# Optimization experiments

Hardware: AMD Instinct MI355X
Metric: run time of the kernel (lower is better)

The kernel has to match this reference:

```python
import jax, jax.numpy as jnp
import numpy as np

N_NODES = 200000
N_EDGES = 800000
N_MOL = 10000
IN_DIM, HDIM, EDGE_DIM = 40, 64, 16
BN_EPS = 1e-5


def _bn_eval(h, gamma, beta, mean, var):
    # BatchNorm1d in eval mode (running stats)
    return gamma * (h - mean) * jax.lax.rsqrt(var + BN_EPS) + beta


def _gine(x, src, dst, edge_attr, We, be, W, b, gamma, beta, mean, var):
    # GINEConv (eps=0): agg_i = sum_{(j->i)} relu(x_j + lin_e(e_ji)); h = nn(x + agg)
    msg = jax.nn.relu(x[src] + edge_attr @ We.T + be)          # [E, d]
    agg = jax.ops.segment_sum(msg, dst, num_segments=x.shape[0])
    h = (x + agg) @ W.T + b                                    # Linear
    h = _bn_eval(h, gamma, beta, mean, var)                    # BatchNorm1d
    return jax.nn.leaky_relu(h)                                # LeakyReLU(0.01); Dropout is identity in eval


def setup_inputs() -> dict:
    key = jax.random.key(0)
    ks = jax.random.split(key, 40)
    d = {}
    d['x'] = jax.random.normal(ks[0], (N_NODES, IN_DIM), jnp.float32)
    d['edge_index'] = jax.random.randint(ks[1], (2, N_EDGES), 0, N_NODES, jnp.int32)
    d['edge_attr'] = jax.random.normal(ks[2], (N_EDGES, EDGE_DIM), jnp.float32)
    d['batch'] = jnp.sort(jax.random.randint(ks[3], (N_NODES,), 0, N_MOL, jnp.int32))
    i = 4
    def nrm(shape, scale=0.05):
        nonlocal i
        i += 1
        return jax.random.normal(ks[i - 1], shape, jnp.float32) * scale
    for l, din in ((1, IN_DIM), (2, HDIM), (3, HDIM)):
        d[f'We{l}'] = nrm((din, EDGE_DIM)); d[f'be{l}'] = nrm((din,))
        d[f'W{l}'] = nrm((HDIM, din)); d[f'b{l}'] = nrm((HDIM,))
        d[f'g{l}'] = jnp.ones((HDIM,), jnp.float32); d[f'bb{l}'] = jnp.zeros((HDIM,), jnp.float32)
        d[f'm{l}'] = nrm((HDIM,)); d[f'v{l}'] = jax.random.uniform(ks[i], (HDIM,), jnp.float32, 0.5, 1.5); i += 1
    D4 = 4 * HDIM
    d['Wl1'] = nrm((D4, D4)); d['bl1'] = nrm((D4,))
    d['Wl2'] = nrm((1, D4)); d['bl2'] = nrm((1,))
    return d


def reference(x, edge_index, edge_attr, batch,
              We1, be1, W1, b1, g1, bb1, m1, v1,
              We2, be2, W2, b2, g2, bb2, m2, v2,
              We3, be3, W3, b3, g3, bb3, m3, v3,
              Wl1, bl1, Wl2, bl2):
    src, dst = edge_index[0], edge_index[1]
    h1 = _gine(x, src, dst, edge_attr, We1, be1, W1, b1, g1, bb1, m1, v1)
    h2 = _gine(h1, src, dst, edge_attr, We2, be2, W2, b2, g2, bb2, m2, v2)
    h3 = _gine(h2, src, dst, edge_attr, We3, be3, W3, b3, g3, bb3, m3, v3)
    h_pool = jax.ops.segment_sum(h3, batch, num_segments=N_MOL)   # global_add_pool
    h_pool_ = h_pool[batch]                                       # repeat_interleave by per-mol counts
    h = jnp.concatenate([h1, h2, h3, h_pool_], axis=1)            # [N, 4*hdim]
    h = jax.nn.leaky_relu(h @ Wl1.T + bl1)
    return h @ Wl2.T + bl2                                        # [N, 1]
```

## Files before the change

kernel.cpp:

```cpp
#include <hip/hip_runtime.h>
#include <hip/hip_bf16.h>

#define N_NODES 200000
#define N_EDGES 800000
#define N_MOL   10000
#define HDIM    64
#define EDGE_DIM 16
#define BN_EPS 1e-5f
#define SCAN_BLOCKS ((N_NODES + 255) / 256)

typedef __attribute__((ext_vector_type(8))) short short8;
typedef __attribute__((ext_vector_type(4))) float f32x4;

__device__ __forceinline__ unsigned int pk2(float a, float b) {
    __hip_bfloat162 h = __float22bfloat162_rn(make_float2(a, b));
    union { __hip_bfloat162 h; unsigned int u; } c;
    c.h = h;
    return c.u;
}
__device__ __forceinline__ short8 cvt8(float4 a, float4 b) {
    union { short8 s; unsigned int u[4]; } r;
    r.u[0] = pk2(a.x, a.y); r.u[1] = pk2(a.z, a.w);
    r.u[2] = pk2(b.x, b.y); r.u[3] = pk2(b.z, b.w);
    return r.s;
}
__device__ __forceinline__ float bf2f(unsigned short u) {
    return __uint_as_float(((unsigned int)u) << 16);
}
__device__ __forceinline__ unsigned short f2bf(float a) {
    union { __hip_bfloat16 h; unsigned short u; } c;
    c.h = __float2bfloat16(a);
    return c.u;
}
__device__ __forceinline__ float4 bf4f(ushort4 u) {
    return make_float4(bf2f(u.x), bf2f(u.y), bf2f(u.z), bf2f(u.w));
}

__global__ __launch_bounds__(256) void cvtx_kernel(
    const float* __restrict__ x, unsigned short* __restrict__ xb)
{
    int i = blockIdx.x * 256 + threadIdx.x;
    if ((size_t)i * 4 >= (size_t)N_NODES * 40) return;
    float4 v = *(const float4*)(x + (size_t)i * 4);
    union { ushort4 s; unsigned int u[2]; } r;
    r.u[0] = pk2(v.x, v.y); r.u[1] = pk2(v.z, v.w);
    *(ushort4*)(xb + (size_t)i * 4) = r.s;
}

__global__ __launch_bounds__(256) void hist_kernel(
    const int* __restrict__ ei, int* __restrict__ counts)
{
    int e = blockIdx.x * 256 + threadIdx.x;
    if (e < N_EDGES) atomicAdd(&counts[ei[N_EDGES + e]], 1);
}

__global__ __launch_bounds__(256) void scan_phase_a(
    const int* __restrict__ counts,
    int* __restrict__ row_ptr, int* __restrict__ block_sums)
{
    __shared__ int lds[256];
    int t = threadIdx.x;
    int i = blockIdx.x * 256 + t;
    int v = (i < N_NODES) ? counts[i] : 0;
    lds[t] = v;
    __syncthreads();
    for (int off = 1; off < 256; off <<= 1) {
        int u = (t >= off) ? lds[t - off] : 0;
        __syncthreads();
        lds[t] += u;
        __syncthreads();
    }
    if (i < N_NODES) row_ptr[i] = lds[t] - v;
    if (t == 255) block_sums[blockIdx.x] = lds[255];
}

__global__ __launch_bounds__(1024) void scan_phase_b(
    int* __restrict__ block_sums)
{
    __shared__ int lds[1024];
    int t = threadIdx.x;
    int v = (t < SCAN_BLOCKS) ? block_sums[t] : 0;
    lds[t] = v;
    __syncthreads();
    for (int off = 1; off < 1024; off <<= 1) {
        int u = (t >= off) ? lds[t - off] : 0;
        __syncthreads();
        lds[t] += u;
        __syncthreads();
    }
    if (t < SCAN_BLOCKS) block_sums[t] = lds[t] - v;
}

__global__ __launch_bounds__(256) void scan_phase_c(
    const int* __restrict__ block_sums,
    int* __restrict__ row_ptr, int* __restrict__ cursor)
{
    int i = blockIdx.x * 256 + threadIdx.x;
    if (i < N_NODES) {
        int v = row_ptr[i] + block_sums[blockIdx.x];
        row_ptr[i] = v;
        cursor[i] = v;
    }
    if (i == 0) row_ptr[N_NODES] = N_EDGES;
}

__global__ __launch_bounds__(256) void scatter_kernel(
    const int* __restrict__ ei, int* __restrict__ cursor,
    int* __restrict__ src_sorted, int* __restrict__ eid_sorted)
{
    int e = blockIdx.x * 256 + threadIdx.x;
    if (e >= N_EDGES) return;
    int d = ei[N_EDGES + e];
    int pos = atomicAdd(&cursor[d], 1);
    src_sorted[pos] = ei[e];
    eid_sorted[pos] = e;
}

#define EMSG_WAVES 8192
template<int DIN>
__global__ __launch_bounds__(256) void emsg_mfma(
    const float* __restrict__ ea,
    const int*   __restrict__ eid_sorted,
    const float* __restrict__ We,
    const float* __restrict__ be,
    unsigned short* __restrict__ emsg)
{
    constexpr int NFT = (DIN + 15) / 16;
    int lane = threadIdx.x & 63;
    int wv = blockIdx.x * 4 + (threadIdx.x >> 6);
    int r = lane & 15, g = lane >> 4;
    const short8 zero8 = (short8){0, 0, 0, 0, 0, 0, 0, 0};

    short8 af[NFT];
    float4 bb[NFT];
    bool   sv[NFT];
#pragma unroll
    for (int ft = 0; ft < NFT; ft++) {
        int feat = ft * 16 + r;
        if (g < 2 && feat < DIN) {
            const float4* w4 = (const float4*)(We + feat * 16 + g * 8);
            af[ft] = cvt8(w4[0], w4[1]);
        } else {
            af[ft] = zero8;
        }
        int feat0 = ft * 16 + g * 4;
        sv[ft] = (feat0 < DIN);
        bb[ft] = sv[ft] ? *(const float4*)(be + feat0)
                        : make_float4(0.f, 0.f, 0.f, 0.f);
    }

    const int NT = N_EDGES / 16;
#pragma unroll 1
    for (int tile = wv; tile < NT; tile += EMSG_WAVES) {
        int j0 = tile * 16;
        int e = eid_sorted[j0 + r];
        short8 zf = zero8;
        if (g < 2) {
            const float4* ep = (const float4*)(ea + (size_t)e * 16 + g * 8);
            zf = cvt8(ep[0], ep[1]);
        }
#pragma unroll
        for (int ft = 0; ft < NFT; ft++) {
            f32x4 acc = (f32x4){0.f, 0.f, 0.f, 0.f};
            acc = __builtin_amdgcn_mfma_f32_16x16x32_bf16(af[ft], zf, acc, 0, 0, 0);
            if (sv[ft]) {
                ushort4 st;
                st.x = f2bf(acc[0] + bb[ft].x);
                st.y = f2bf(acc[1] + bb[ft].y);
                st.z = f2bf(acc[2] + bb[ft].z);
                st.w = f2bf(acc[3] + bb[ft].w);
                *(ushort4*)(emsg + (size_t)(j0 + r) * DIN + ft * 16 + g * 4) = st;
            }
        }
    }
}

template<int DIN>
__global__ __launch_bounds__(256) void agg_pre(
    const unsigned short* __restrict__ feat,
    const int*   __restrict__ row_ptr,
    const int*   __restrict__ src_sorted,
    const unsigned short* __restrict__ emsg,
    unsigned short* __restrict__ AGGb)
{
    int lane = threadIdx.x & 63;
    int wv = blockIdx.x * 4 + (threadIdx.x >> 6);
    int n0 = wv * 8;
    if (n0 >= N_NODES) return;
    int eg = lane >> 4;
    int f4 = lane & 15;
    const bool vf = (f4 * 4 < DIN);
    const int f4c = vf ? f4 : 0;

    int lo = row_ptr[n0];
#pragma unroll 1
    for (int ni = 0; ni < 8; ni++) {
        int node = n0 + ni;
        int hi = row_ptr[node + 1];
        float4 acc = {0.f, 0.f, 0.f, 0.f};
#pragma unroll 1
        for (int j0 = lo; j0 < hi; j0 += 4) {
            int j = j0 + eg;
            bool ev = (j < hi);
            int jc = ev ? j : (hi - 1);
            int s = src_sorted[jc];
            ushort4 xu = *(const ushort4*)(feat + (size_t)s * DIN + f4c * 4);
            ushort4 mu = *(const ushort4*)(emsg + (size_t)jc * DIN + f4c * 4);
            float4 xv = bf4f(xu), mv = bf4f(mu);
            float t0 = fmaxf(xv.x + mv.x, 0.f);
            float t1 = fmaxf(xv.y + mv.y, 0.f);
            float t2 = fmaxf(xv.z + mv.z, 0.f);
            float t3 = fmaxf(xv.w + mv.w, 0.f);
            if (ev && vf) {
                acc.x += t0; acc.y += t1; acc.z += t2; acc.w += t3;
            }
        }
        acc.x += __shfl_xor(acc.x, 16, 64);
        acc.y += __shfl_xor(acc.y, 16, 64);
        acc.z += __shfl_xor(acc.z, 16, 64);
        acc.w += __shfl_xor(acc.w, 16, 64);
        acc.x += __shfl_xor(acc.x, 32, 64);
        acc.y += __shfl_xor(acc.y, 32, 64);
        acc.z += __shfl_xor(acc.z, 32, 64);
        acc.w += __shfl_xor(acc.w, 32, 64);
        if (eg == 0) {
            float4 xd = {0.f, 0.f, 0.f, 0.f};
            if (vf) xd = bf4f(*(const ushort4*)(feat + (size_t)node * DIN + f4 * 4));
            float4 o = vf ? make_float4(acc.x + xd.x, acc.y + xd.y,
                                        acc.z + xd.z, acc.w + xd.w)
                          : make_float4(0.f, 0.f, 0.f, 0.f);
            ushort4 st;
            st.x = f2bf(o.x); st.y = f2bf(o.y);
            st.z = f2bf(o.z); st.w = f2bf(o.w);
            *(ushort4*)(AGGb + (size_t)node * HDIM + f4 * 4) = st;
        }
        lo = hi;
    }
}

template<int DIN>
__global__ __launch_bounds__(256) void agg_kernel(
    const unsigned short* __restrict__ feat,
    const int*   __restrict__ row_ptr,
    const int*   __restrict__ src_sorted,
    const int*   __restrict__ eid_sorted,
    const float* __restrict__ ea,
    const float* __restrict__ We,
    const float* __restrict__ be,
    unsigned short* __restrict__ AGGb)
{
    int lane = threadIdx.x & 63;
    int wv = __builtin_amdgcn_readfirstlane(blockIdx.x * 4 + (threadIdx.x >> 6));
    int n0 = wv * 8;
    if (n0 >= N_NODES) return;
    int f = lane;

    float wrow[16];
    float bias = 0.f;
    if (f < DIN) {
#pragma unroll
        for (int j = 0; j < 16; j++) wrow[j] = We[f * 16 + j];
        bias = be[f];
    } else {
#pragma unroll
        for (int j = 0; j < 16; j++) wrow[j] = 0.f;
    }

    int lo = row_ptr[n0];
    int hi = row_ptr[n0 + 8];
    int cur = 0;
    int nb = row_ptr[n0 + 1];
    float acc = 0.f;

    for (int j0 = lo; j0 < hi; j0 += 8) {
        int jn = min(8, hi - j0);
        int s[8], e[8];
#pragma unroll
        for (int k = 0; k < 8; k++) {
            int j = min(j0 + k, hi - 1);
            s[k] = src_sorted[j];
            e[k] = eid_sorted[j];
        }
        float xv[8];
#pragma unroll
        for (int k = 0; k < 8; k++)
            xv[k] = (f < DIN) ? bf2f(feat[(size_t)s[k] * DIN + f]) : 0.f;

#pragma unroll
        for (int k = 0; k < 8; k++) {
            if (k >= jn) break;
            int j = j0 + k;
            while (j >= nb) {
                float xd = (f < DIN) ? bf2f(feat[(size_t)(n0 + cur) * DIN + f]) : 0.f;
                AGGb[(size_t)(n0 + cur) * HDIM + f] = f2bf(acc + xd);
                acc = 0.f;
                cur++;
                nb = row_ptr[n0 + cur + 1];
            }
            const float4* ep = (const float4*)(ea + (size_t)e[k] * 16);
            float4 q0 = ep[0], q1 = ep[1], q2 = ep[2], q3 = ep[3];
            float a = bias;
            a = fmaf(q0.x, wrow[0],  a); a = fmaf(q0.y, wrow[1],  a);
            a = fmaf(q0.z, wrow[2],  a); a = fmaf(q0.w, wrow[3],  a);
            a = fmaf(q1.x, wrow[4],  a); a = fmaf(q1.y, wrow[5],  a);
            a = fmaf(q1.z, wrow[6],  a); a = fmaf(q1.w, wrow[7],  a);
            a = fmaf(q2.x, wrow[8],  a); a = fmaf(q2.y, wrow[9],  a);
            a = fmaf(q2.z, wrow[10], a); a = fmaf(q2.w, wrow[11], a);
            a = fmaf(q3.x, wrow[12], a); a = fmaf(q3.y, wrow[13], a);
            a = fmaf(q3.z, wrow[14], a); a = fmaf(q3.w, wrow[15], a);
            acc += fmaxf(xv[k] + a, 0.f);
        }
    }
    while (cur < 8) {
        float xd = (f < DIN) ? bf2f(feat[(size_t)(n0 + cur) * DIN + f]) : 0.f;
        AGGb[(size_t)(n0 + cur) * HDIM + f] = f2bf(acc + xd);
        acc = 0.f;
        cur++;
    }
}

template<int DIN>
__global__ __launch_bounds__(256) void node_mfma(
    const unsigned short* __restrict__ AGGb,
    unsigned short* __restrict__ Hb,
    const float* __restrict__ W,
    const float* __restrict__ bias,
    const float* __restrict__ gam,
    const float* __restrict__ bet,
    const float* __restrict__ mean,
    const float* __restrict__ var)
{
    int lane = threadIdx.x & 63;
    int wave = blockIdx.x * 4 + (threadIdx.x >> 6);
    if (wave >= N_NODES / 64) return;
    int n0 = wave * 64;
    int r = lane & 15;
    int g = lane >> 4;

    const short8 zero8 = (short8){0, 0, 0, 0, 0, 0, 0, 0};

    short8 zf[4][2];
#pragma unroll
    for (int nt = 0; nt < 4; nt++) {
        int node = n0 + nt * 16 + r;
        const unsigned short* ar = AGGb + (size_t)node * HDIM;
        zf[nt][0] = *(const short8*)(ar + g * 8);
        zf[nt][1] = *(const short8*)(ar + 32 + g * 8);
    }

    const float4* b4  = (const float4*)bias;
    const float4* g4  = (const float4*)gam;
    const float4* be4 = (const float4*)bet;
    const float4* m4  = (const float4*)mean;
    const float4* v4  = (const float4*)var;

#pragma unroll
    for (int ft = 0; ft < 4; ft++) {
        const float* wr = W + (size_t)(ft * 16 + r) * DIN;
        short8 af[2];
        {
            float4 w0 = *(const float4*)(wr + g * 8);
            float4 w1 = *(const float4*)(wr + g * 8 + 4);
            af[0] = cvt8(w0, w1);
            if (DIN == 64) {
                w0 = *(const float4*)(wr + 32 + g * 8);
                w1 = *(const float4*)(wr + 36 + g * 8);
                af[1] = cvt8(w0, w1);
            } else if (g == 0) {
                w0 = *(const float4*)(wr + 32);
                w1 = *(const float4*)(wr + 36);
                af[1] = cvt8(w0, w1);
            } else {
                af[1] = zero8;
            }
        }

        f32x4 acc[4];
#pragma unroll
        for (int nt = 0; nt < 4; nt++) acc[nt] = (f32x4){0.f, 0.f, 0.f, 0.f};

#pragma unroll
        for (int ks = 0; ks < 2; ks++) {
#pragma unroll
            for (int nt = 0; nt < 4; nt++) {
                acc[nt] = __builtin_amdgcn_mfma_f32_16x16x32_bf16(
                    af[ks], zf[nt][ks], acc[nt], 0, 0, 0);
            }
        }

        int idx = ft * 4 + g;
        float4 bb = b4[idx], gg = g4[idx], bt = be4[idx], mm = m4[idx], vv = v4[idx];
        float s0 = gg.x * rsqrtf(vv.x + BN_EPS);
        float s1 = gg.y * rsqrtf(vv.y + BN_EPS);
        float s2 = gg.z * rsqrtf(vv.z + BN_EPS);
        float s3 = gg.w * rsqrtf(vv.w + BN_EPS);
#pragma unroll
        for (int nt = 0; nt < 4; nt++) {
            int node = n0 + nt * 16 + r;
            float y0 = s0 * (acc[nt][0] + bb.x - mm.x) + bt.x;
            float y1 = s1 * (acc[nt][1] + bb.y - mm.y) + bt.y;
            float y2 = s2 * (acc[nt][2] + bb.z - mm.z) + bt.z;
            float y3 = s3 * (acc[nt][3] + bb.w - mm.w) + bt.w;
            y0 = (y0 > 0.f) ? y0 : 0.01f * y0;
            y1 = (y1 > 0.f) ? y1 : 0.01f * y1;
            y2 = (y2 > 0.f) ? y2 : 0.01f * y2;
            y3 = (y3 > 0.f) ? y3 : 0.01f * y3;
            union { uint2 v; unsigned int u[2]; } st;
            st.u[0] = pk2(y0, y1);
            st.u[1] = pk2(y2, y3);
            *(uint2*)(Hb + (size_t)node * HDIM + ft * 16 + g * 4) = st.v;
        }
    }
}

__global__ __launch_bounds__(256) void pool_kernel(
    const unsigned short* __restrict__ h3b,
    const int*   __restrict__ batch,
    float*       __restrict__ hpool)
{
    int gid = blockIdx.x * 256 + threadIdx.x;
    if (gid >= N_NODES * HDIM) return;
    int i = gid >> 6, f = gid & 63;
    atomicAdd(&hpool[(size_t)batch[i] * HDIM + f], bf2f(h3b[gid]));
}

__global__ __launch_bounds__(256, 2) void head_kernel(
    const unsigned short* __restrict__ h1b,
    const unsigned short* __restrict__ h2b,
    const unsigned short* __restrict__ h3b,
    const float* __restrict__ hpool,
    const int*   __restrict__ batch,
    const float* __restrict__ Wl1, const float* __restrict__ bl1,
    const float* __restrict__ Wl2, const float* __restrict__ bl2,
    float*       __restrict__ out)
{
    __shared__ short8 wlds[2048];

    int tid = threadIdx.x;
    int lane = tid & 63;
    int wave = blockIdx.x * 4 + (tid >> 6);
    bool active = (wave < N_NODES / 64);
    int n0 = active ? wave * 64 : (N_NODES - 64);
    int r = lane & 15;
    int g = lane >> 4;

    short8 zf[4][8];
#pragma unroll
    for (int nt = 0; nt < 4; nt++) {
        int node = n0 + nt * 16 + r;
        const unsigned short* r1 = h1b + (size_t)node * 64;
        const unsigned short* r2 = h2b + (size_t)node * 64;
        const unsigned short* r3 = h3b + (size_t)node * 64;
        const float* rp = hpool + (size_t)batch[node] * 64;
        zf[nt][0] = *(const short8*)(r1 + g * 8);
        zf[nt][1] = *(const short8*)(r1 + 32 + g * 8);
        zf[nt][2] = *(const short8*)(r2 + g * 8);
        zf[nt][3] = *(const short8*)(r2 + 32 + g * 8);
        zf[nt][4] = *(const short8*)(r3 + g * 8);
        zf[nt][5] = *(const short8*)(r3 + 32 + g * 8);
        const float4* q;
        q = (const float4*)(rp + g * 8);        zf[nt][6] = cvt8(q[0], q[1]);
        q = (const float4*)(rp + 32 + g * 8);   zf[nt][7] = cvt8(q[0], q[1]);
    }

    float p[4] = {0.f, 0.f, 0.f, 0.f};
    const float4* bl1_4 = (const float4*)bl1;
    const float4* wl2_4 = (const float4*)Wl2;

#pragma unroll 1
    for (int pass = 0; pass < 4; pass++) {
        if (pass) __syncthreads();
#pragma unroll
        for (int i = 0; i < 8; i++) {
            int local = tid + i * 256;
            int ftq = local >> 9;
            int ks  = (local >> 6) & 7;
            int lf  = local & 63;
            int rr = lf & 15, gg = lf >> 4;
            int ft = pass * 4 + ftq;
            const float4* q = (const float4*)(Wl1 + (size_t)(ft * 16 + rr) * 256
                                              + ks * 32 + gg * 8);
            wlds[local] = cvt8(q[0], q[1]);
        }
        __syncthreads();

#pragma unroll 1
        for (int ftq = 0; ftq < 4; ftq++) {
            int ft = pass * 4 + ftq;
            short8 af[8];
#pragma unroll
            for (int ks = 0; ks < 8; ks++) af[ks] = wlds[(ftq * 8 + ks) * 64 + lane];

            f32x4 acc[4];
#pragma unroll
            for (int nt = 0; nt < 4; nt++) acc[nt] = (f32x4){0.f, 0.f, 0.f, 0.f};
#pragma unroll
            for (int ks = 0; ks < 8; ks++) {
#pragma unroll
                for (int nt = 0; nt < 4; nt++) {
                    acc[nt] = __builtin_amdgcn_mfma_f32_16x16x32_bf16(
                        af[ks], zf[nt][ks], acc[nt], 0, 0, 0);
                }
            }

            float4 bl = bl1_4[ft * 4 + g];
            float4 w2 = wl2_4[ft * 4 + g];
#pragma unroll
            for (int nt = 0; nt < 4; nt++) {
                float a0 = acc[nt][0] + bl.x;
                float a1 = acc[nt][1] + bl.y;
                float a2 = acc[nt][2] + bl.z;
                float a3 = acc[nt][3] + bl.w;
                a0 = (a0 > 0.f) ? a0 : 0.01f * a0;
                a1 = (a1 > 0.f) ? a1 : 0.01f * a1;
                a2 = (a2 > 0.f) ? a2 : 0.01f * a2;
                a3 = (a3 > 0.f) ? a3 : 0.01f * a3;
                p[nt] += w2.x * a0 + w2.y * a1 + w2.z * a2 + w2.w * a3;
            }
        }
    }

    float b2 = bl2[0];
#pragma unroll
    for (int nt = 0; nt < 4; nt++) {
        float s = p[nt];
        s += __shfl_xor(s, 16, 64);
        s += __shfl_xor(s, 32, 64);
        if (g == 0 && active) out[n0 + nt * 16 + r] = s + b2;
    }
}

extern "C" void kernel_launch(void* const* d_in, const int* in_sizes, int n_in,
                              void* d_out, int out_size, void* d_ws, size_t ws_size,
                              hipStream_t stream) {
    const float* x     = (const float*)d_in[0];
    const int*   ei    = (const int*)  d_in[1];
    const float* ea    = (const float*)d_in[2];
    const int*   batch = (const int*)  d_in[3];

    const float* We1 = (const float*)d_in[4];  const float* be1 = (const float*)d_in[5];
    const float* W1  = (const float*)d_in[6];  const float* b1  = (const float*)d_in[7];
    const float* g1  = (const float*)d_in[8];  const float* bb1 = (const float*)d_in[9];
    const float* m1  = (const float*)d_in[10]; const float* v1  = (const float*)d_in[11];

    const float* We2 = (const float*)d_in[12]; const float* be2 = (const float*)d_in[13];
    const float* W2  = (const float*)d_in[14]; const float* b2  = (const float*)d_in[15];
    const float* g2  = (const float*)d_in[16]; const float* bb2 = (const float*)d_in[17];
    const float* m2  = (const float*)d_in[18]; const float* v2  = (const float*)d_in[19];

    const float* We3 = (const float*)d_in[20]; const float* be3 = (const float*)d_in[21];
    const float* W3  = (const float*)d_in[22]; const float* b3  = (const float*)d_in[23];
    const float* g3  = (const float*)d_in[24]; const float* bb3 = (const float*)d_in[25];
    const float* m3  = (const float*)d_in[26]; const float* v3  = (const float*)d_in[27];

    const float* Wl1 = (const float*)d_in[28]; const float* bl1 = (const float*)d_in[29];
    const float* Wl2 = (const float*)d_in[30]; const float* bl2 = (const float*)d_in[31];

    float* out = (float*)d_out;

    char* wp = (char*)d_ws;
    auto carve = [&](size_t bytes) -> char* {
        char* r = wp;
        wp += (bytes + 255) & ~(size_t)255;
        return r;
    };
    unsigned short* AGGb  = (unsigned short*)carve((size_t)N_NODES * HDIM * 2);
    unsigned short* xb    = (unsigned short*)carve((size_t)N_NODES * 40 * 2);
    unsigned short* Hb1   = (unsigned short*)carve((size_t)N_NODES * HDIM * 2);
    unsigned short* Hb2   = (unsigned short*)carve((size_t)N_NODES * HDIM * 2);
    unsigned short* Hb3   = (unsigned short*)carve((size_t)N_NODES * HDIM * 2);
    float* hpool          = (float*)         carve((size_t)N_MOL * HDIM * 4);
    int* counts           = (int*)           carve((size_t)N_NODES * 4);
    int* row_ptr          = (int*)           carve((size_t)(N_NODES + 1) * 4);
    int* cursor           = (int*)           carve((size_t)N_NODES * 4);
    int* src_sorted       = (int*)           carve((size_t)N_EDGES * 4);
    int* eid_sorted       = (int*)           carve((size_t)N_EDGES * 4);
    int* block_sums       = (int*)           carve((size_t)SCAN_BLOCKS * 4);
    unsigned short* emsg  = (unsigned short*)carve((size_t)N_EDGES * HDIM * 2);
    size_t need           = (size_t)(wp - (char*)d_ws);
    bool use_pre = (ws_size >= need);

    hipMemsetAsync(hpool, 0, (size_t)N_MOL * HDIM * sizeof(float), stream);
    hipMemsetAsync(counts, 0, (size_t)N_NODES * sizeof(int), stream);

    dim3 blk(256);
    dim3 cgrid(((size_t)N_NODES * 40 / 4 + 255) / 256);
    dim3 egrid(N_EDGES / 256);
    dim3 mgrid(EMSG_WAVES / 4);
    dim3 sgrid(SCAN_BLOCKS);
    dim3 agrid((N_NODES / 8) / 4);
    dim3 ngrid((N_NODES / 64 + 3) / 4);
    dim3 pgrid((N_NODES * HDIM) / 256);
    dim3 hgrid((N_NODES / 64 + 3) / 4);

    cvtx_kernel<<<cgrid, blk, 0, stream>>>(x, xb);
    hist_kernel<<<egrid, blk, 0, stream>>>(ei, counts);
    scan_phase_a<<<sgrid, blk, 0, stream>>>(counts, row_ptr, block_sums);
    scan_phase_b<<<1, 1024, 0, stream>>>(block_sums);
    scan_phase_c<<<sgrid, blk, 0, stream>>>(block_sums, row_ptr, cursor);
    scatter_kernel<<<egrid, blk, 0, stream>>>(ei, cursor, src_sorted, eid_sorted);

    if (use_pre) {
        emsg_mfma<40><<<mgrid, blk, 0, stream>>>(ea, eid_sorted, We1, be1, emsg);
        agg_pre<40><<<agrid, blk, 0, stream>>>(xb, row_ptr, src_sorted, emsg, AGGb);
        node_mfma<40><<<ngrid, blk, 0, stream>>>(AGGb, Hb1, W1, b1, g1, bb1, m1, v1);
        emsg_mfma<64><<<mgrid, blk, 0, stream>>>(ea, eid_sorted, We2, be2, emsg);
        agg_pre<64><<<agrid, blk, 0, stream>>>(Hb1, row_ptr, src_sorted, emsg, AGGb);
        node_mfma<64><<<ngrid, blk, 0, stream>>>(AGGb, Hb2, W2, b2, g2, bb2, m2, v2);
        emsg_mfma<64><<<mgrid, blk, 0, stream>>>(ea, eid_sorted, We3, be3, emsg);
        agg_pre<64><<<agrid, blk, 0, stream>>>(Hb2, row_ptr, src_sorted, emsg, AGGb);
        node_mfma<64><<<ngrid, blk, 0, stream>>>(AGGb, Hb3, W3, b3, g3, bb3, m3, v3);
    } else {
        agg_kernel<40><<<agrid, blk, 0, stream>>>(xb, row_ptr, src_sorted, eid_sorted,
                                                  ea, We1, be1, AGGb);
        node_mfma<40><<<ngrid, blk, 0, stream>>>(AGGb, Hb1, W1, b1, g1, bb1, m1, v1);
        agg_kernel<64><<<agrid, blk, 0, stream>>>(Hb1, row_ptr, src_sorted, eid_sorted,
                                                  ea, We2, be2, AGGb);
        node_mfma<64><<<ngrid, blk, 0, stream>>>(AGGb, Hb2, W2, b2, g2, bb2, m2, v2);
        agg_kernel<64><<<agrid, blk, 0, stream>>>(Hb2, row_ptr, src_sorted, eid_sorted,
                                                  ea, We3, be3, AGGb);
        node_mfma<64><<<ngrid, blk, 0, stream>>>(AGGb, Hb3, W3, b3, g3, bb3, m3, v3);
    }

    pool_kernel<<<pgrid, blk, 0, stream>>>(Hb3, batch, hpool);
    head_kernel<<<hgrid, blk, 0, stream>>>(Hb1, Hb2, Hb3, hpool, batch,
                                           Wl1, bl1, Wl2, bl2, out);
}
```

Baseline: 580.5 us.

## Fuse three per-layer edge-message GEMMs into one kernel with separate buffers

Replaces three per-layer emsg_mfma launches with a single emsg_all kernel. It gathers each edge's attributes once and computes the edge-linear outputs for all three GINE layers, writing them to three separate bf16 buffers (layer 1 stored with stride 40). This removes two redundant gathers of edge_attr and eid_sorted plus two launches. In exchange it needs more workspace (extra N_EDGES*(40+64) bf16) and more registers for the weight fragments, and it only runs when the workspace is large enough.

```diff
diff --git a/kernel.cpp b/kernel.cpp
--- a/kernel.cpp
+++ b/kernel.cpp
@@ -117,6 +117,97 @@
 }
 
 #define EMSG_WAVES 8192
+__global__ __launch_bounds__(256) void emsg_all(
+    const float* __restrict__ ea,
+    const int*   __restrict__ eid_sorted,
+    const float* __restrict__ We1, const float* __restrict__ be1,
+    const float* __restrict__ We2, const float* __restrict__ be2,
+    const float* __restrict__ We3, const float* __restrict__ be3,
+    unsigned short* __restrict__ em1,
+    unsigned short* __restrict__ em2,
+    unsigned short* __restrict__ em3)
+{
+    int lane = threadIdx.x & 63;
+    int wv = blockIdx.x * 4 + (threadIdx.x >> 6);
+    int r = lane & 15, g = lane >> 4;
+    const short8 zero8 = (short8){0, 0, 0, 0, 0, 0, 0, 0};
+
+    short8 af1[3]; float4 bb1v[3]; bool sv1[3];
+#pragma unroll
+    for (int ft = 0; ft < 3; ft++) {
+        int feat = ft * 16 + r;
+        if (g < 2 && feat < 40) {
+            const float4* w4 = (const float4*)(We1 + feat * 16 + g * 8);
+            af1[ft] = cvt8(w4[0], w4[1]);
+        } else af1[ft] = zero8;
+        int feat0 = ft * 16 + g * 4;
+        sv1[ft] = (feat0 < 40);
+        bb1v[ft] = sv1[ft] ? *(const float4*)(be1 + feat0)
+                           : make_float4(0.f, 0.f, 0.f, 0.f);
+    }
+    short8 af2[4], af3[4]; float4 bb2v[4], bb3v[4];
+#pragma unroll
+    for (int ft = 0; ft < 4; ft++) {
+        int feat = ft * 16 + r;
+        if (g < 2) {
+            const float4* w4 = (const float4*)(We2 + feat * 16 + g * 8);
+            af2[ft] = cvt8(w4[0], w4[1]);
+            w4 = (const float4*)(We3 + feat * 16 + g * 8);
+            af3[ft] = cvt8(w4[0], w4[1]);
+        } else { af2[ft] = zero8; af3[ft] = zero8; }
+        int feat0 = ft * 16 + g * 4;
+        bb2v[ft] = *(const float4*)(be2 + feat0);
+        bb3v[ft] = *(const float4*)(be3 + feat0);
+    }
+
+    const int NT = N_EDGES / 16;
+#pragma unroll 1
+    for (int tile = wv; tile < NT; tile += EMSG_WAVES) {
+        int j0 = tile * 16;
+        int e = eid_sorted[j0 + r];
+        short8 zf = zero8;
+        if (g < 2) {
+            const float4* ep = (const float4*)(ea + (size_t)e * 16 + g * 8);
+            zf = cvt8(ep[0], ep[1]);
+        }
+#pragma unroll
+        for (int ft = 0; ft < 3; ft++) {
+            f32x4 acc = (f32x4){0.f, 0.f, 0.f, 0.f};
+            acc = __builtin_amdgcn_mfma_f32_16x16x32_bf16(af1[ft], zf, acc, 0, 0, 0);
+            if (sv1[ft]) {
+                ushort4 st;
+                st.x = f2bf(acc[0] + bb1v[ft].x);
+                st.y = f2bf(acc[1] + bb1v[ft].y);
+                st.z = f2bf(acc[2] + bb1v[ft].z);
+                st.w = f2bf(acc[3] + bb1v[ft].w);
+                *(ushort4*)(em1 + (size_t)(j0 + r) * 40 + ft * 16 + g * 4) = st;
+            }
+        }
+#pragma unroll
+        for (int ft = 0; ft < 4; ft++) {
+            f32x4 acc = (f32x4){0.f, 0.f, 0.f, 0.f};
+            acc = __builtin_amdgcn_mfma_f32_16x16x32_bf16(af2[ft], zf, acc, 0, 0, 0);
+            ushort4 st;
+            st.x = f2bf(acc[0] + bb2v[ft].x);
+            st.y = f2bf(acc[1] + bb2v[ft].y);
+            st.z = f2bf(acc[2] + bb2v[ft].z);
+            st.w = f2bf(acc[3] + bb2v[ft].w);
+            *(ushort4*)(em2 + (size_t)(j0 + r) * 64 + ft * 16 + g * 4) = st;
+        }
+#pragma unroll
+        for (int ft = 0; ft < 4; ft++) {
+            f32x4 acc = (f32x4){0.f, 0.f, 0.f, 0.f};
+            acc = __builtin_amdgcn_mfma_f32_16x16x32_bf16(af3[ft], zf, acc, 0, 0, 0);
+            ushort4 st;
+            st.x = f2bf(acc[0] + bb3v[ft].x);
+            st.y = f2bf(acc[1] + bb3v[ft].y);
+            st.z = f2bf(acc[2] + bb3v[ft].z);
+            st.w = f2bf(acc[3] + bb3v[ft].w);
+            *(ushort4*)(em3 + (size_t)(j0 + r) * 64 + ft * 16 + g * 4) = st;
+        }
+    }
+}
+
 template<int DIN>
 __global__ __launch_bounds__(256) void emsg_mfma(
     const float* __restrict__ ea,
@@ -576,9 +667,13 @@
     int* src_sorted       = (int*)           carve((size_t)N_EDGES * 4);
     int* eid_sorted       = (int*)           carve((size_t)N_EDGES * 4);
     int* block_sums       = (int*)           carve((size_t)SCAN_BLOCKS * 4);
-    unsigned short* emsg  = (unsigned short*)carve((size_t)N_EDGES * HDIM * 2);
-    size_t need           = (size_t)(wp - (char*)d_ws);
-    bool use_pre = (ws_size >= need);
+    unsigned short* emsgA = (unsigned short*)carve((size_t)N_EDGES * HDIM * 2);
+    size_t need_pre       = (size_t)(wp - (char*)d_ws);
+    unsigned short* em1   = (unsigned short*)carve((size_t)N_EDGES * 40 * 2);
+    unsigned short* em3   = (unsigned short*)carve((size_t)N_EDGES * HDIM * 2);
+    size_t need_fused     = (size_t)(wp - (char*)d_ws);
+    bool use_fused = (ws_size >= need_fused);
+    bool use_pre   = (ws_size >= need_pre);
 
     hipMemsetAsync(hpool, 0, (size_t)N_MOL * HDIM * sizeof(float), stream);
     hipMemsetAsync(counts, 0, (size_t)N_NODES * sizeof(int), stream);
@@ -600,15 +695,24 @@
     scan_phase_c<<<sgrid, blk, 0, stream>>>(block_sums, row_ptr, cursor);
     scatter_kernel<<<egrid, blk, 0, stream>>>(ei, cursor, src_sorted, eid_sorted);
 
-    if (use_pre) {
-        emsg_mfma<40><<<mgrid, blk, 0, stream>>>(ea, eid_sorted, We1, be1, emsg);
-        agg_pre<40><<<agrid, blk, 0, stream>>>(xb, row_ptr, src_sorted, emsg, AGGb);
+    if (use_fused) {
+        emsg_all<<<mgrid, blk, 0, stream>>>(ea, eid_sorted, We1, be1, We2, be2,
+                                            We3, be3, em1, emsgA, em3);
+        agg_pre<40><<<agrid, blk, 0, stream>>>(xb, row_ptr, src_sorted, em1, AGGb);
         node_mfma<40><<<ngrid, blk, 0, stream>>>(AGGb, Hb1, W1, b1, g1, bb1, m1, v1);
-        emsg_mfma<64><<<mgrid, blk, 0, stream>>>(ea, eid_sorted, We2, be2, emsg);
-        agg_pre<64><<<agrid, blk, 0, stream>>>(Hb1, row_ptr, src_sorted, emsg, AGGb);
+        agg_pre<64><<<agrid, blk, 0, stream>>>(Hb1, row_ptr, src_sorted, emsgA, AGGb);
         node_mfma<64><<<ngrid, blk, 0, stream>>>(AGGb, Hb2, W2, b2, g2, bb2, m2, v2);
-        emsg_mfma<64><<<mgrid, blk, 0, stream>>>(ea, eid_sorted, We3, be3, emsg);
-        agg_pre<64><<<agrid, blk, 0, stream>>>(Hb2, row_ptr, src_sorted, emsg, AGGb);
+        agg_pre<64><<<agrid, blk, 0, stream>>>(Hb2, row_ptr, src_sorted, em3, AGGb);
+        node_mfma<64><<<ngrid, blk, 0, stream>>>(AGGb, Hb3, W3, b3, g3, bb3, m3, v3);
+    } else if (use_pre) {
+        emsg_mfma<40><<<mgrid, blk, 0, stream>>>(ea, eid_sorted, We1, be1, emsgA);
+        agg_pre<40><<<agrid, blk, 0, stream>>>(xb, row_ptr, src_sorted, emsgA, AGGb);
+        node_mfma<40><<<ngrid, blk, 0, stream>>>(AGGb, Hb1, W1, b1, g1, bb1, m1, v1);
+        emsg_mfma<64><<<mgrid, blk, 0, stream>>>(ea, eid_sorted, We2, be2, emsgA);
+        agg_pre<64><<<agrid, blk, 0, stream>>>(Hb1, row_ptr, src_sorted, emsgA, AGGb);
+        node_mfma<64><<<ngrid, blk, 0, stream>>>(AGGb, Hb2, W2, b2, g2, bb2, m2, v2);
+        emsg_mfma<64><<<mgrid, blk, 0, stream>>>(ea, eid_sorted, We3, be3, emsgA);
+        agg_pre<64><<<agrid, blk, 0, stream>>>(Hb2, row_ptr, src_sorted, emsgA, AGGb);
         node_mfma<64><<<ngrid, blk, 0, stream>>>(AGGb, Hb3, W3, b3, g3, bb3, m3, v3);
     } else {
         agg_kernel<40><<<agrid, blk, 0, stream>>>(xb, row_ptr, src_sorted, eid_sorted,
```

New measurement: 571.6 us. No clear change (-1.5%).
